# Kernel optimization log

Measured on AMD Instinct MI355X. Metric: run time of the kernel, lower is better.

The kernel has to match this reference:

```python
import jax, jax.numpy as jnp
import numpy as np

B, N, L, D, H, DH = 1, 512, 256, 256, 8, 32  # batch, n_seqs, length, d_msa, heads, d_hidden
EPS = 1e-5


def setup_inputs() -> dict:
    key = jax.random.key(0)
    ks = jax.random.split(key, 3)
    msa = jax.random.normal(ks[0], (B, N, L, D), dtype=jnp.float32)
    # xavier-uniform-ish scale for (H*DH, D) linear weights
    lim = float(np.sqrt(6.0 / (D + H * DH)))
    Wq = jax.random.uniform(ks[1], (H * DH, D), minval=-lim, maxval=lim, dtype=jnp.float32)
    Wk = jax.random.uniform(ks[2], (H * DH, D), minval=-lim, maxval=lim, dtype=jnp.float32)
    return {
        "msa": msa,
        "Wq": Wq,
        "bq": jnp.zeros((H * DH,), jnp.float32),
        "Wk": Wk,
        "bk": jnp.zeros((H * DH,), jnp.float32),
        "ln_gamma": jnp.ones((D,), jnp.float32),
        "ln_beta": jnp.zeros((D,), jnp.float32),
        "stride": 0,
    }


def reference(msa, Wq, bq, Wk, bk, ln_gamma, ln_beta, stride):
    # stride only controls chunking in the original (no math effect); ignored.
    def ln(x):
        m = jnp.mean(x, axis=-1, keepdims=True)
        v = jnp.mean((x - m) ** 2, axis=-1, keepdims=True)
        return (x - m) * jax.lax.rsqrt(v + EPS) * ln_gamma + ln_beta

    scale = 1.0 / np.sqrt(DH)
    b, n, l = msa.shape[:3]
    # query from target (first) sequence: (B, L, H, DH)
    q = (ln(msa[:, 0]) @ Wq.T + bq).reshape(b, l, H, DH) * scale
    # keys from all sequences: (B, N, L, H, DH)
    k = (ln(msa) @ Wk.T + bk).reshape(b, n, l, H, DH)
    # attention logits over the sequence axis N: (B, N, L, H)
    logits = jnp.einsum("blhd,bnlhd->bnlh", q, k)
    attn = jax.nn.softmax(logits, axis=1)
    # dropout is identity in eval mode
    return attn[..., None]  # (B, N, L, H, 1)
```

## Files before the change

### kernel.cpp

```cpp
#include <hip/hip_runtime.h>
#include <hip/hip_bf16.h>
#include <cstdint>

#define LL 256
#define NN 512
#define DD 256
#define HH 8
#define EPSF 1e-5f
#define WGS 264

typedef __attribute__((ext_vector_type(8))) __bf16 bf16x8;
typedef __attribute__((ext_vector_type(4))) float f32x4;

static __device__ __forceinline__ void lb_sync() {
    __builtin_amdgcn_sched_barrier(0);
    asm volatile("s_waitcnt lgkmcnt(0)" ::: "memory");
    __builtin_amdgcn_s_barrier();
    __builtin_amdgcn_sched_barrier(0);
}

static __device__ __forceinline__ void load_group(
    const float* __restrict__ msa, int l, int row0, int col, int kb, float4 (&buf)[16])
{
    const float* rp = msa + ((size_t)(row0 + col) * LL + l) * DD + (kb << 3);
    #pragma unroll
    for (int ks = 0; ks < 8; ++ks) {
        buf[2 * ks]     = *(const float4*)(rp + ks * 32);
        buf[2 * ks + 1] = *(const float4*)(rp + ks * 32 + 4);
    }
}

static __device__ __forceinline__ void compute_group(
    const float4 (&buf)[16], const bf16x8 (&bfr)[8], f32x4& hacc, f32x4& gacc)
{
    #pragma unroll
    for (int ks = 0; ks < 8; ++ks) {
        float4 u = buf[2 * ks], v = buf[2 * ks + 1];
        bf16x8 a;
        a[0] = (__bf16)u.x; a[1] = (__bf16)u.y; a[2] = (__bf16)u.z; a[3] = (__bf16)u.w;
        a[4] = (__bf16)v.x; a[5] = (__bf16)v.y; a[6] = (__bf16)v.z; a[7] = (__bf16)v.w;
        hacc = __builtin_amdgcn_mfma_f32_16x16x32_bf16(a, bfr[ks], hacc, 0, 0, 0);
        gacc = __builtin_amdgcn_mfma_f32_16x16x32_bf16(a, a,       gacc, 0, 0, 0);
    }
}

static __device__ __forceinline__ void store_group(
    int nloc0, int col, int kb, const f32x4& hacc, const f32x4& gacc,
    float* logits, float* sS, float* sQ)
{
    #pragma unroll
    for (int i = 0; i < 4; ++i) {
        int n = nloc0 + (kb << 2) + i;
        if (col < HH)       logits[col * NN + n] = hacc[i];
        else if (col == HH) sS[n] = hacc[i];
    }
    if (kb == (col >> 2)) sQ[nloc0 + col] = gacc[col & 3];
}

__global__ __launch_bounds__(1024, 4) void k_fused(
    const float* __restrict__ msa, const float* __restrict__ Wq,
    const float* __restrict__ bq, const float* __restrict__ Wk,
    const float* __restrict__ gamma, const float* __restrict__ beta,
    float* __restrict__ out)
{
    const int l = blockIdx.x;
    const int tid = threadIdx.x, wave = tid >> 6, lane = tid & 63;
    const int col = lane & 15, kb = lane >> 4;

    __shared__ __align__(16) float logits[HH * NN];
    __shared__ __align__(16) float sS[NN];
    __shared__ __align__(16) float sQ[NN];
    __shared__ __align__(16) __bf16 WgL[16 * WGS];
    __shared__ __align__(16) float qpart[4][264];
    __shared__ float lnx[DD];
    __shared__ float qv[DD];
    __shared__ float red8[8];
    __shared__ float stats[16];
    __shared__ float Gs[HH];

    float4 A[16];
    load_group(msa, l, wave * 16, col, kb, A);

    {
        float x0 = (tid < DD) ? msa[(size_t)l * DD + tid] : 0.f;
        float s = x0, ss = x0 * x0;
        #pragma unroll
        for (int m = 32; m >= 1; m >>= 1) { s += __shfl_xor(s, m); ss += __shfl_xor(ss, m); }
        if (tid < DD && lane == 0) { red8[wave * 2] = s; red8[wave * 2 + 1] = ss; }
        lb_sync();
        if (tid < DD) {
            float sm = red8[0] + red8[2] + red8[4] + red8[6];
            float sq = red8[1] + red8[3] + red8[5] + red8[7];
            float mean = sm * (1.f / DD);
            float var  = sq * (1.f / DD) - mean * mean;
            float rs   = rsqrtf(var + EPSF);
            lnx[tid] = (x0 - mean) * rs * gamma[tid] + beta[tid];
        }
        lb_sync();
        {
            const int r = tid & 255, qtr = tid >> 8;
            const float4* wr = (const float4*)(Wq + (size_t)r * DD) + qtr * 16;
            const float* lx = lnx + qtr * 64;
            float acc = 0.f;
            #pragma unroll 4
            for (int j = 0; j < 16; ++j) {
                float4 w4 = wr[j];
                acc += lx[4*j] * w4.x + lx[4*j+1] * w4.y + lx[4*j+2] * w4.z + lx[4*j+3] * w4.w;
            }
            qpart[qtr][r] = acc;
        }
        lb_sync();
        if (tid < DD)
            qv[tid] = (qpart[0][tid] + qpart[1][tid] + qpart[2][tid] + qpart[3][tid]
                       + bq[tid]) * 0.17677669529663687f;
        lb_sync();
        {
            const int c = tid & 255, hb = tid >> 8;
            const float gm = gamma[c];
            #pragma unroll
            for (int hi = 0; hi < 2; ++hi) {
                int h = hb + hi * 4;
                float a = 0.f;
                const float* wk = Wk + ((size_t)h * 32) * DD + c;
                #pragma unroll 8
                for (int d = 0; d < 32; ++d)
                    a += qv[h * 32 + d] * wk[(size_t)d * DD];
                WgL[h * WGS + c] = (__bf16)(gm * a);
            }
        }
        if (tid < DD) {
            WgL[8 * WGS + tid] = (__bf16)1.0f;
            #pragma unroll
            for (int h = 9; h < 16; ++h) WgL[h * WGS + tid] = (__bf16)0.0f;
        }
        lb_sync();
        if (wave < HH) {
            float gsum = 0.f;
            #pragma unroll
            for (int i = 0; i < 4; ++i) gsum += (float)WgL[wave * WGS + lane * 4 + i];
            #pragma unroll
            for (int m = 32; m >= 1; m >>= 1) gsum += __shfl_xor(gsum, m);
            if (lane == 0) Gs[wave] = gsum;
        }
        lb_sync();
    }

    bf16x8 bfr[8];
    #pragma unroll
    for (int ks = 0; ks < 8; ++ks)
        bfr[ks] = *(const bf16x8*)&WgL[col * WGS + ks * 32 + kb * 8];

    const f32x4 z = {0.f, 0.f, 0.f, 0.f};
    {
        f32x4 ha = z, ga = z;
        compute_group(A, bfr, ha, ga);
        store_group(wave * 16, col, kb, ha, ga, logits, sS, sQ);
    }
    load_group(msa, l, 256 + wave * 16, col, kb, A);
    {
        f32x4 ha = z, ga = z;
        compute_group(A, bfr, ha, ga);
        store_group(256 + wave * 16, col, kb, ha, ga, logits, sS, sQ);
    }
    lb_sync();

    if (wave < HH) {
        const int h = wave;
        const float Gh = Gs[h];
        const float* lp = logits + h * NN;
        float4 ra = ((const float4*)lp)[lane * 2];
        float4 rb = ((const float4*)lp)[lane * 2 + 1];
        float4 sa = ((const float4*)sS)[lane * 2];
        float4 sb = ((const float4*)sS)[lane * 2 + 1];
        float4 qa = ((const float4*)sQ)[lane * 2];
        float4 qb = ((const float4*)sQ)[lane * 2 + 1];
        float raw[8] = {ra.x, ra.y, ra.z, ra.w, rb.x, rb.y, rb.z, rb.w};
        float sv[8]  = {sa.x, sa.y, sa.z, sa.w, sb.x, sb.y, sb.z, sb.w};
        float qv2[8] = {qa.x, qa.y, qa.z, qa.w, qb.x, qb.y, qb.z, qb.w};
        float adj[8];
        #pragma unroll
        for (int i = 0; i < 8; ++i) {
            float mean = sv[i] * (1.f / DD);
            float var  = qv2[i] * (1.f / DD) - mean * mean;
            float rs   = rsqrtf(var + EPSF);
            adj[i] = rs * (raw[i] - mean * Gh);
        }
        float mx = adj[0];
        #pragma unroll
        for (int i = 1; i < 8; ++i) mx = fmaxf(mx, adj[i]);
        #pragma unroll
        for (int m = 32; m >= 1; m >>= 1) mx = fmaxf(mx, __shfl_xor(mx, m));
        float sm = 0.f;
        #pragma unroll
        for (int i = 0; i < 8; ++i) sm += __expf(adj[i] - mx);
        #pragma unroll
        for (int m = 32; m >= 1; m >>= 1) sm += __shfl_xor(sm, m);
        if (lane == 0) { stats[wave] = mx; stats[8 + wave] = 1.f / sm; }
    }
    lb_sync();

    if (tid < NN) {
        const int n = tid;
        float s = sS[n], q2 = sQ[n];
        float mean = s * (1.f / DD);
        float var  = q2 * (1.f / DD) - mean * mean;
        float rs   = rsqrtf(var + EPSF);
        float o[8];
        #pragma unroll
        for (int h = 0; h < HH; ++h) {
            float adj = rs * (logits[h * NN + n] - mean * Gs[h]);
            o[h] = __expf(adj - stats[h]) * stats[8 + h];
        }
        float* op = out + (size_t)n * LL * HH + (size_t)l * HH;
        float4 p0 = {o[0], o[1], o[2], o[3]};
        float4 p1 = {o[4], o[5], o[6], o[7]};
        *(float4*)(op)     = p0;
        *(float4*)(op + 4) = p1;
    }
}

extern "C" void kernel_launch(void* const* d_in, const int* in_sizes, int n_in,
                              void* d_out, int out_size, void* d_ws, size_t ws_size,
                              hipStream_t stream) {
    (void)in_sizes; (void)n_in; (void)out_size; (void)d_ws; (void)ws_size;
    const float* msa   = (const float*)d_in[0];
    const float* Wq    = (const float*)d_in[1];
    const float* bq    = (const float*)d_in[2];
    const float* Wk    = (const float*)d_in[3];
    const float* gamma = (const float*)d_in[5];
    const float* beta  = (const float*)d_in[6];
    k_fused<<<dim3(LL), dim3(1024), 0, stream>>>(msa, Wq, bq, Wk, gamma, beta, (float*)d_out);
}
```

Measured before the change: 41.07 us.

## Prefetch half of second MSA row group into LDS via async global_load_lds

```diff
diff --git a/kernel.cpp b/kernel.cpp
--- a/kernel.cpp
+++ b/kernel.cpp
@@ -67,19 +67,31 @@
     const int tid = threadIdx.x, wave = tid >> 6, lane = tid & 63;
     const int col = lane & 15, kb = lane >> 4;
 
+    __shared__ __align__(16) float tile[128 * 256];
     __shared__ __align__(16) float logits[HH * NN];
     __shared__ __align__(16) float sS[NN];
     __shared__ __align__(16) float sQ[NN];
     __shared__ __align__(16) __bf16 WgL[16 * WGS];
-    __shared__ __align__(16) float qpart[4][264];
     __shared__ float lnx[DD];
     __shared__ float qv[DD];
     __shared__ float red8[8];
     __shared__ float stats[16];
     __shared__ float Gs[HH];
 
-    float4 A[16];
-    load_group(msa, l, wave * 16, col, kb, A);
+    if (wave < 8) {
+        #pragma unroll
+        for (int r = 0; r < 16; ++r) {
+            const int n = 256 + wave * 16 + r;
+            const char* g = (const char*)(msa + ((size_t)n * LL + l) * DD)
+                            + (((lane * 16) ^ ((r & 7) << 4)));
+            __builtin_amdgcn_global_load_lds(
+                (const __attribute__((address_space(1))) void*)g,
+                (__attribute__((address_space(3))) void*)
+                    ((char*)(tile + (size_t)(wave * 16 + r) * 256) + lane * 16),
+                16, 0, 0);
+        }
+    }
+    __builtin_amdgcn_sched_barrier(0);
 
     {
         float x0 = (tid < DD) ? msa[(size_t)l * DD + tid] : 0.f;
@@ -107,12 +119,14 @@
                 float4 w4 = wr[j];
                 acc += lx[4*j] * w4.x + lx[4*j+1] * w4.y + lx[4*j+2] * w4.z + lx[4*j+3] * w4.w;
             }
-            qpart[qtr][r] = acc;
-        }
-        lb_sync();
-        if (tid < DD)
-            qv[tid] = (qpart[0][tid] + qpart[1][tid] + qpart[2][tid] + qpart[3][tid]
-                       + bq[tid]) * 0.17677669529663687f;
+            float* qpart = logits;
+            qpart[qtr * 264 + r] = acc;
+            lb_sync();
+            if (tid < DD)
+                qv[tid] = (qpart[0 * 264 + tid] + qpart[1 * 264 + tid]
+                         + qpart[2 * 264 + tid] + qpart[3 * 264 + tid]
+                         + bq[tid]) * 0.17677669529663687f;
+        }
         lb_sync();
         {
             const int c = tid & 255, hb = tid >> 8;
@@ -151,13 +165,33 @@
         bfr[ks] = *(const bf16x8*)&WgL[col * WGS + ks * 32 + kb * 8];
 
     const f32x4 z = {0.f, 0.f, 0.f, 0.f};
+    float4 A[16];
+    load_group(msa, l, wave * 16, col, kb, A);
     {
         f32x4 ha = z, ga = z;
         compute_group(A, bfr, ha, ga);
         store_group(wave * 16, col, kb, ha, ga, logits, sS, sQ);
     }
-    load_group(msa, l, 256 + wave * 16, col, kb, A);
-    {
+
+    if (wave < 8) {
+        asm volatile("s_waitcnt vmcnt(0)" ::: "memory");
+        __builtin_amdgcn_sched_barrier(0);
+        f32x4 ha = z, ga = z;
+        const char* tb = (const char*)(tile + (size_t)(wave * 16 + col) * 256);
+        const int swz = (col & 7) << 4;
+        #pragma unroll
+        for (int ks = 0; ks < 8; ++ks) {
+            float4 u = *(const float4*)(tb + ((ks * 128 + kb * 32) ^ swz));
+            float4 v = *(const float4*)(tb + ((ks * 128 + kb * 32 + 16) ^ swz));
+            bf16x8 a;
+            a[0] = (__bf16)u.x; a[1] = (__bf16)u.y; a[2] = (__bf16)u.z; a[3] = (__bf16)u.w;
+            a[4] = (__bf16)v.x; a[5] = (__bf16)v.y; a[6] = (__bf16)v.z; a[7] = (__bf16)v.w;
+            ha = __builtin_amdgcn_mfma_f32_16x16x32_bf16(a, bfr[ks], ha, 0, 0, 0);
+            ga = __builtin_amdgcn_mfma_f32_16x16x32_bf16(a, a,       ga, 0, 0, 0);
+        }
+        store_group(256 + wave * 16, col, kb, ha, ga, logits, sS, sQ);
+    } else {
+        load_group(msa, l, 256 + wave * 16, col, kb, A);
         f32x4 ha = z, ga = z;
         compute_group(A, bfr, ha, ga);
         store_group(256 + wave * 16, col, kb, ha, ga, logits, sS, sQ);
```

Result: no change. 41.12 us (+0.1%).
